# Performance work log

Hardware: AMD Instinct MI355X
Metric: run time of the kernel (lower is better)

## Reference

```python
import jax, jax.numpy as jnp
import numpy as np

TWO_PI = 2.0 * np.pi
EPS = 1e-12  # torch F.normalize eps


def setup_inputs() -> dict:
    key = jax.random.key(0)
    ks = jax.random.split(key, 12)
    B, NS, G = 16, 128, 20000
    P, S, E, T = 200, 128, 128, 50
    return {
        "x_genes": jax.random.normal(ks[0], (B, NS, G), jnp.float32),
        "tissue_idx": jax.random.randint(ks[1], (B, NS), 0, T, jnp.int32),
        "pathway_idx": jax.random.randint(ks[2], (P, S), 0, G, jnp.int32),
        "W_proj": jax.random.normal(ks[3], (P, E, S), jnp.float32) * (1.0 / np.sqrt(S)),
        "b_proj": jax.random.normal(ks[4], (P, E), jnp.float32) * 0.02,
        "tissue_table": jax.random.normal(ks[5], (T, E), jnp.float32),
        "W1": jax.random.normal(ks[6], (E, 32), jnp.float32) * (1.0 / np.sqrt(E)),
        "b1": jax.random.normal(ks[7], (32,), jnp.float32) * 0.02,
        "W2": jax.random.normal(ks[8], (32, 2), jnp.float32) * (1.0 / np.sqrt(32)),
        "b2": jax.random.normal(ks[9], (2,), jnp.float32) * 0.02,
        "Wdec": jax.random.normal(ks[10], (2, G), jnp.float32) * (1.0 / np.sqrt(2.0)),
        "bdec": jax.random.normal(ks[11], (G,), jnp.float32) * 0.02,
    }


def _l2norm(v):
    n = jnp.sqrt(jnp.sum(v * v, axis=-1, keepdims=True))
    return v / jnp.maximum(n, EPS)


def reference(x_genes, tissue_idx, pathway_idx, W_proj, b_proj, tissue_table,
              W1, b1, W2, b2, Wdec, bdec):
    B, NS, G = x_genes.shape
    x = x_genes.reshape(-1, G)            # [N, G], N = B*NS
    t = tissue_idx.reshape(-1)            # [N]

    # Pathway tokenizer: gather gene subsets + per-pathway linear (grouped GEMM)
    xg = x[:, pathway_idx]                # [N, P, S]
    H = jax.nn.relu(jnp.einsum('nps,pes->npe', xg, W_proj) + b_proj)  # [N, P, E]

    # Single-query attention with tissue embedding as query
    Q = tissue_table[t]                   # [N, E]
    scale = 1.0 / np.sqrt(H.shape[-1])
    scores = jnp.einsum('ne,npe->np', Q, H) * scale   # [N, P]
    attn = jax.nn.softmax(scores, axis=-1)
    context = jnp.einsum('np,npe->ne', attn, H)       # [N, E]

    # to_latent MLP (dropout=0 / eval)
    h = jax.nn.relu(context @ W1 + b1)
    pc = h @ W2 + b2                      # [N, 2]
    pcn = _l2norm(pc)
    ang = jnp.remainder(jnp.arctan2(pcn[:, 1], pcn[:, 0]) + TWO_PI, TWO_PI)

    # decode + normalize
    rec = _l2norm(pcn @ Wdec + bdec)      # [N, G]

    return (pcn.reshape(B, NS, 2), ang.reshape(B, NS), rec.reshape(B, NS, G))
```

## Files before the change

### kernel.cpp

```cpp
#include <hip/hip_runtime.h>
#include <cmath>

#define GG 20000
#define NN 2048
#define PP 200
#define SS 128
#define EE 128
#define TN 128
#define TPP 8
#define NOCT 25

typedef __bf16 bf16x8 __attribute__((ext_vector_type(8)));
typedef float f32x16 __attribute__((ext_vector_type(16)));
typedef unsigned short u16x8 __attribute__((ext_vector_type(8)));

__device__ __align__(16) unsigned g_xTi[(size_t)GG * NN];
__device__ __align__(16) unsigned short g_Wsw[(size_t)PP * 32768];
__device__ float g_ctxp[(size_t)NN * NOCT * EE];
__device__ float g_mT[NOCT * NN];
__device__ float g_lT[NOCT * NN];
__device__ float g_statsp[6][64];
__device__ float g_stats[8];

__device__ __forceinline__ unsigned short f2bf(float f) {
  unsigned u = __builtin_bit_cast(unsigned, f);
  return (unsigned short)((u + 0x7FFFu + ((u >> 16) & 1u)) >> 16);
}
__device__ __forceinline__ float bf2f(unsigned short h) {
  return __builtin_bit_cast(float, (unsigned)h << 16);
}
__device__ __forceinline__ unsigned packhl(float f) {
  unsigned short h = f2bf(f);
  unsigned short l = f2bf(f - bf2f(h));
  return (unsigned)h | ((unsigned)l << 16);
}

__global__ __launch_bounds__(256) void transpose_convert_kernel(
    const float* __restrict__ x)
{
  __shared__ unsigned tile[128 * 129];
  const int g0 = blockIdx.x * 128;
  const int n0 = blockIdx.y * 128;
  const int t = threadIdx.x;

  {
    const int gq = t & 31, nr = t >> 5;
    const int g = g0 + gq * 4;
    #pragma unroll
    for (int k = 0; k < 16; ++k) {
      int nl = nr + 8 * k;
      unsigned v0 = 0, v1 = 0, v2 = 0, v3 = 0;
      if (g + 3 < GG) {
        float4 v = *(const float4*)&x[(size_t)(n0 + nl) * GG + g];
        v0 = packhl(v.x); v1 = packhl(v.y); v2 = packhl(v.z); v3 = packhl(v.w);
      }
      unsigned* row = &tile[nl * 129 + gq * 4];
      row[0] = v0; row[1] = v1; row[2] = v2; row[3] = v3;
    }
  }
  __syncthreads();
  {
    const int nq = t & 31, gr = t >> 5;
    #pragma unroll
    for (int k = 0; k < 16; ++k) {
      int gl = gr + 8 * k;
      int g = g0 + gl;
      if (g < GG) {
        uint4 o;
        o.x = tile[(nq * 4 + 0) * 129 + gl];
        o.y = tile[(nq * 4 + 1) * 129 + gl];
        o.z = tile[(nq * 4 + 2) * 129 + gl];
        o.w = tile[(nq * 4 + 3) * 129 + gl];
        *(uint4*)&g_xTi[(size_t)g * NN + n0 + nq * 4] = o;
      }
    }
  }
}

__global__ __launch_bounds__(256) void wconvert_kernel(const float* __restrict__ Wp)
{
  unsigned v = blockIdx.x * 256 + threadIdx.x;
  const int si = v & 7;
  const int slp = (v >> 3) & 7;
  const int e = (v >> 6) & 127;
  const int ch = (v >> 13) & 1;
  const int p = v >> 14;
  const int slot = slp ^ (e & 7);
  const int s = ch * 64 + slot * 8 + si;
  float f = Wp[((size_t)p * EE + e) * SS + s];
  unsigned short h = f2bf(f);
  unsigned short l = f2bf(f - bf2f(h));
  size_t base = (size_t)(p * 2 + ch) * 16384 + e * 64 + slp * 8 + si;
  g_Wsw[base] = h;
  g_Wsw[base + 8192] = l;
}

__global__ __launch_bounds__(256) void wdec_stats_partial(
    const float* __restrict__ Wdec, const float* __restrict__ bdec)
{
  __shared__ float red[6][4];
  const int b = blockIdx.x;
  const int start = b * 313;
  const int end = (start + 313 < GG) ? start + 313 : GG;
  float s00 = 0, s11 = 0, s01 = 0, t0 = 0, t1 = 0, sbb = 0;
  for (int g = start + threadIdx.x; g < end; g += 256) {
    float w0 = Wdec[g], w1 = Wdec[GG + g], bb = bdec[g];
    s00 += w0 * w0; s11 += w1 * w1; s01 += w0 * w1;
    t0 += w0 * bb;  t1 += w1 * bb;  sbb += bb * bb;
  }
  #pragma unroll
  for (int off = 32; off >= 1; off >>= 1) {
    s00 += __shfl_xor(s00, off); s11 += __shfl_xor(s11, off);
    s01 += __shfl_xor(s01, off); t0 += __shfl_xor(t0, off);
    t1 += __shfl_xor(t1, off);   sbb += __shfl_xor(sbb, off);
  }
  const int w = threadIdx.x >> 6;
  if ((threadIdx.x & 63) == 0) {
    red[0][w] = s00; red[1][w] = s11; red[2][w] = s01;
    red[3][w] = t0;  red[4][w] = t1;  red[5][w] = sbb;
  }
  __syncthreads();
  if (threadIdx.x < 6)
    g_statsp[threadIdx.x][b] = red[threadIdx.x][0] + red[threadIdx.x][1] +
                               red[threadIdx.x][2] + red[threadIdx.x][3];
}

__global__ __launch_bounds__(64) void wdec_stats_final()
{
  const int t = threadIdx.x;
  #pragma unroll
  for (int k = 0; k < 6; ++k) {
    float v = g_statsp[k][t];
    #pragma unroll
    for (int off = 32; off >= 1; off >>= 1) v += __shfl_xor(v, off);
    if (t == 0) g_stats[k] = v;
  }
}

__device__ __forceinline__ void load16(unsigned* xr, const int* sidx_lds,
                                       int sbase, int kh, int ncol) {
  #pragma unroll
  for (int ks2 = 0; ks2 < 2; ++ks2)
    #pragma unroll
    for (int j = 0; j < 8; ++j) {
      int s = (sbase + ks2) * 16 + kh * 8 + j;
      xr[ks2 * 8 + j] = g_xTi[(size_t)sidx_lds[s] * NN + ncol];
    }
}

__device__ __forceinline__ void compute2ks(const unsigned short* wb,
                                           const unsigned* xr, f32x16 (&acc)[4],
                                           int ksbase, int nl, int kh) {
  #pragma unroll
  for (int ks2 = 0; ks2 < 2; ++ks2) {
    const int ks = ksbase + ks2;
    const unsigned short* wAh = wb + (ks >> 2) * 16384;
    const unsigned short* wAl = wAh + 8192;
    u16x8 bhu, blu;
    #pragma unroll
    for (int j = 0; j < 8; ++j) {
      unsigned v = xr[ks2 * 8 + j];
      bhu[j] = (unsigned short)(v & 0xffffu);
      blu[j] = (unsigned short)(v >> 16);
    }
    bf16x8 bh = __builtin_bit_cast(bf16x8, bhu);
    bf16x8 bl = __builtin_bit_cast(bf16x8, blu);
    #pragma unroll
    for (int et = 0; et < 4; ++et) {
      const int e = et * 32 + nl;
      const int slp = ((ks & 3) * 2 + kh) ^ (e & 7);
      bf16x8 ah = __builtin_bit_cast(bf16x8, *(const uint4*)(wAh + e * 64 + slp * 8));
      bf16x8 al = __builtin_bit_cast(bf16x8, *(const uint4*)(wAl + e * 64 + slp * 8));
      acc[et] = __builtin_amdgcn_mfma_f32_32x32x16_bf16(ah, bh, acc[et], 0, 0, 0);
      acc[et] = __builtin_amdgcn_mfma_f32_32x32x16_bf16(ah, bl, acc[et], 0, 0, 0);
      acc[et] = __builtin_amdgcn_mfma_f32_32x32x16_bf16(al, bh, acc[et], 0, 0, 0);
    }
  }
}

__device__ __forceinline__ void pathway_body(
    int p, unsigned short* wbuf, int* sidx, float* sbp,
    const int* __restrict__ pidx, const float* __restrict__ bp,
    const float* __restrict__ tt, int tid_n,
    int t, int w, int ln, int nl, int kh, int ncol,
    f32x16 (&h)[4], float& s_out)
{
  __syncthreads();
  if (t < 128) sidx[t] = pidx[p * SS + t];
  else         sbp[t - 128] = bp[p * EE + (t - 128)];
  {
    const unsigned short* src = g_Wsw + (size_t)p * 32768 + w * 8192 + ln * 8;
    unsigned short* dst = wbuf + w * 8192;
    #pragma unroll
    for (int j = 0; j < 16; ++j) {
      __builtin_amdgcn_global_load_lds(
          (const __attribute__((address_space(1))) unsigned int*)(src + j * 512),
          (__attribute__((address_space(3))) unsigned int*)(dst + j * 512), 16, 0, 0);
    }
  }
  __syncthreads();

  #pragma unroll
  for (int et = 0; et < 4; ++et)
    #pragma unroll
    for (int r = 0; r < 16; ++r) h[et][r] = 0.f;

  unsigned xa[16], xb[16];
  load16(xa, sidx, 0, kh, ncol);
  load16(xb, sidx, 2, kh, ncol);
  compute2ks(wbuf, xa, h, 0, nl, kh);
  load16(xa, sidx, 4, kh, ncol);
  compute2ks(wbuf, xb, h, 2, nl, kh);
  load16(xb, sidx, 6, kh, ncol);
  compute2ks(wbuf, xa, h, 4, nl, kh);
  compute2ks(wbuf, xb, h, 6, nl, kh);

  const float4* qp = (const float4*)(tt + (size_t)tid_n * EE);
  float scr = 0.f;
  #pragma unroll
  for (int et = 0; et < 4; ++et)
    #pragma unroll
    for (int rq = 0; rq < 4; ++rq) {
      int e0 = et * 32 + rq * 8 + kh * 4;
      float4 q4 = qp[e0 >> 2];
      float4 b4 = *(const float4*)&sbp[e0];
      float h0 = fmaxf(h[et][rq * 4 + 0] + b4.x, 0.f);
      float h1 = fmaxf(h[et][rq * 4 + 1] + b4.y, 0.f);
      float h2 = fmaxf(h[et][rq * 4 + 2] + b4.z, 0.f);
      float h3 = fmaxf(h[et][rq * 4 + 3] + b4.w, 0.f);
      h[et][rq * 4 + 0] = h0; h[et][rq * 4 + 1] = h1;
      h[et][rq * 4 + 2] = h2; h[et][rq * 4 + 3] = h3;
      scr += h0 * q4.x + h1 * q4.y + h2 * q4.z + h3 * q4.w;
    }
  scr += __shfl_xor(scr, 32);
  s_out = scr * 0.08838834764831845f;
}

__global__ __launch_bounds__(256, 2) void proj_mfma_kernel(
    const int* __restrict__ tidx, const int* __restrict__ pidx,
    const float* __restrict__ bp, const float* __restrict__ tt)
{
  __shared__ __align__(16) unsigned short wbuf[32768];
  __shared__ int sidx[SS];
  __shared__ float sbp[EE];

  const int t = threadIdx.x;
  const int w = t >> 6;
  const int ln = t & 63;
  const int nl = ln & 31;
  const int kh = ln >> 5;
  const int n0 = blockIdx.x * TN;
  const int oct = blockIdx.y;
  const int ncol = n0 + w * 32 + nl;
  const int tid_n = tidx[ncol];

  f32x16 ctx[4];
  #pragma unroll
  for (int et = 0; et < 4; ++et)
    #pragma unroll
    for (int r = 0; r < 16; ++r) ctx[et][r] = 0.f;
  float m_r = -1e30f, l_r = 0.f;

  f32x16 h[4];
  float s;
  for (int pp = 0; pp < TPP; ++pp) {
    pathway_body(oct * TPP + pp, wbuf, sidx, sbp, pidx, bp, tt, tid_n,
                 t, w, ln, nl, kh, ncol, h, s);
    const float mn = fmaxf(m_r, s);
    const float f = expf(m_r - mn);
    const float wg = expf(s - mn);
    l_r = l_r * f + wg;
    m_r = mn;
    #pragma unroll
    for (int et = 0; et < 4; ++et)
      #pragma unroll
      for (int r = 0; r < 16; ++r)
        ctx[et][r] = ctx[et][r] * f + wg * h[et][r];
  }

  __syncthreads();
  float* tb = ((float*)wbuf) + w * (32 * 128);
  #pragma unroll
  for (int et = 0; et < 4; ++et)
    #pragma unroll
    for (int rq = 0; rq < 4; ++rq) {
      int slot = et * 8 + rq * 2 + kh;
      float4 v = make_float4(ctx[et][rq * 4 + 0], ctx[et][rq * 4 + 1],
                             ctx[et][rq * 4 + 2], ctx[et][rq * 4 + 3]);
      *(float4*)&tb[nl * 128 + ((slot ^ nl) << 2)] = v;
    }
  __syncthreads();
  {
    const int rrow = ln >> 1, eh = (ln & 1) * 16;
    const int nn = n0 + w * 32 + rrow;
    float* dst = g_ctxp + ((size_t)nn * NOCT + oct) * EE + eh * 4;
    const float* srcrow = tb + rrow * 128;
    #pragma unroll
    for (int k = 0; k < 16; ++k) {
      int slot = eh + k;
      *(float4*)&dst[k * 4] = *(const float4*)&srcrow[(slot ^ rrow) << 2];
    }
  }
  if (ln < 32) {
    g_mT[oct * NN + ncol] = m_r;
    g_lT[oct * NN + ncol] = l_r;
  }
}

__global__ __launch_bounds__(256) void combine_rec_kernel(
    const float* __restrict__ W1, const float* __restrict__ b1,
    const float* __restrict__ W2, const float* __restrict__ b2,
    const float* __restrict__ Wdec, const float* __restrict__ bdec,
    float* __restrict__ out)
{
  const int n = blockIdx.x;
  const int t = threadIdx.x;
  __shared__ float ws[NOCT];
  __shared__ float ctx2[2][EE];
  __shared__ float r1[4], r2[4];
  __shared__ float hsh[32];
  __shared__ float qsh[3];

  float mv = (t < NOCT) ? g_mT[t * NN + n] : -1e30f;
  float lv = (t < NOCT) ? g_lT[t * NN + n] : 0.f;
  float M = mv;
  #pragma unroll
  for (int off = 32; off >= 1; off >>= 1) M = fmaxf(M, __shfl_xor(M, off));
  if ((t & 63) == 0) r1[t >> 6] = M;
  __syncthreads();
  M = fmaxf(fmaxf(r1[0], r1[1]), fmaxf(r1[2], r1[3]));
  float wv = (t < NOCT) ? expf(mv - M) : 0.f;
  if (t < NOCT) ws[t] = wv;
  float Lp = wv * lv;
  #pragma unroll
  for (int off = 32; off >= 1; off >>= 1) Lp += __shfl_xor(Lp, off);
  if ((t & 63) == 0) r2[t >> 6] = Lp;
  __syncthreads();
  const float L = r2[0] + r2[1] + r2[2] + r2[3];

  {
    const int e = t & 127, hf = t >> 7;
    const int sA = hf ? 13 : 0, sB = hf ? NOCT : 13;
    const float* base = g_ctxp + ((size_t)n * NOCT + sA) * EE + e;
    float c = 0.f;
    for (int s = sA; s < sB; ++s) c += ws[s] * base[(size_t)(s - sA) * EE];
    ctx2[hf][e] = c;
  }
  __syncthreads();
  const float invL = 1.f / L;
  if (t < 32) {
    float h = 0.f;
    for (int e = 0; e < EE; ++e) h += (ctx2[0][e] + ctx2[1][e]) * W1[e * 32 + t];
    hsh[t] = fmaxf(h * invL + b1[t], 0.f);
  }
  __syncthreads();
  if (t == 0) {
    float p0 = b2[0], p1 = b2[1];
    #pragma unroll
    for (int k = 0; k < 32; ++k) { p0 += hsh[k] * W2[k * 2]; p1 += hsh[k] * W2[k * 2 + 1]; }
    float invp = 1.f / fmaxf(sqrtf(p0 * p0 + p1 * p1), 1e-12f);
    float q0 = p0 * invp, q1 = p1 * invp;
    const float PI2 = 6.2831853071795864769f;
    float ang = atan2f(q1, q0) + PI2;
    if (ang >= PI2) ang -= PI2;
    out[n * 2 + 0] = q0;
    out[n * 2 + 1] = q1;
    out[2 * NN + n] = ang;
    float n2 = q0 * q0 * g_stats[0] + q1 * q1 * g_stats[1] +
               2.f * q0 * q1 * g_stats[2] +
               2.f * q0 * g_stats[3] + 2.f * q1 * g_stats[4] + g_stats[5];
    qsh[0] = q0;
    qsh[1] = q1;
    qsh[2] = 1.f / fmaxf(sqrtf(n2), 1e-12f);
  }
  __syncthreads();
  const float q0 = qsh[0], q1 = qsh[1], inv = qsh[2];

  float* orec = out + 3 * NN + (size_t)n * GG;
  for (int i = t; i < GG / 4; i += 256) {
    float4 w0 = *(const float4*)&Wdec[i * 4];
    float4 w1 = *(const float4*)&Wdec[GG + i * 4];
    float4 b4 = *(const float4*)&bdec[i * 4];
    float4 o;
    o.x = (q0 * w0.x + q1 * w1.x + b4.x) * inv;
    o.y = (q0 * w0.y + q1 * w1.y + b4.y) * inv;
    o.z = (q0 * w0.z + q1 * w1.z + b4.z) * inv;
    o.w = (q0 * w0.w + q1 * w1.w + b4.w) * inv;
    *(float4*)&orec[i * 4] = o;
  }
}

extern "C" void kernel_launch(void* const* d_in, const int* in_sizes, int n_in,
                              void* d_out, int out_size, void* d_ws, size_t ws_size,
                              hipStream_t stream) {
  (void)in_sizes; (void)n_in; (void)out_size; (void)d_ws; (void)ws_size;
  const float* x    = (const float*)d_in[0];
  const int*   tidx = (const int*)  d_in[1];
  const int*   pidx = (const int*)  d_in[2];
  const float* Wp   = (const float*)d_in[3];
  const float* bp   = (const float*)d_in[4];
  const float* tt   = (const float*)d_in[5];
  const float* W1   = (const float*)d_in[6];
  const float* b1   = (const float*)d_in[7];
  const float* W2   = (const float*)d_in[8];
  const float* b2   = (const float*)d_in[9];
  const float* Wdec = (const float*)d_in[10];
  const float* bdec = (const float*)d_in[11];
  float* out = (float*)d_out;

  dim3 gridT((GG + 127) / 128, NN / 128, 1);
  transpose_convert_kernel<<<gridT, 256, 0, stream>>>(x);
  wconvert_kernel<<<(PP * 16384) / 256, 256, 0, stream>>>(Wp);
  wdec_stats_partial<<<64, 256, 0, stream>>>(Wdec, bdec);
  wdec_stats_final<<<1, 64, 0, stream>>>();

  dim3 gridA(NN / TN, NOCT, 1);
  proj_mfma_kernel<<<gridA, 256, 0, stream>>>(tidx, pidx, bp, tt);

  combine_rec_kernel<<<NN, 256, 0, stream>>>(W1, b1, W2, b2, Wdec, bdec, out);
}
```

Baseline: 290.3 us.

## Halve weight LDS buffer to raise occupancy and fold stats reduction into combine

The projection kernel now stages each pathway's bf16 weights in two 32KB halves instead of one 64KB buffer. This halves LDS use so launch bounds can ask for four blocks per CU instead of two, and the context transpose is split into two phases to fit the smaller buffer. The cost is extra barriers per pathway and less overlap between the x gathers and the MFMAs. Separately, the tiny final stats-reduction kernel is removed and each combine block sums the 64 partials itself, trading one launch for redundant work in every block.

```diff
diff --git a/kernel.cpp b/kernel.cpp
--- a/kernel.cpp
+++ b/kernel.cpp
@@ -20,7 +20,6 @@
 __device__ float g_mT[NOCT * NN];
 __device__ float g_lT[NOCT * NN];
 __device__ float g_statsp[6][64];
-__device__ float g_stats[8];
 
 __device__ __forceinline__ unsigned short f2bf(float f) {
   unsigned u = __builtin_bit_cast(unsigned, f);
@@ -125,18 +124,6 @@
                                red[threadIdx.x][2] + red[threadIdx.x][3];
 }
 
-__global__ __launch_bounds__(64) void wdec_stats_final()
-{
-  const int t = threadIdx.x;
-  #pragma unroll
-  for (int k = 0; k < 6; ++k) {
-    float v = g_statsp[k][t];
-    #pragma unroll
-    for (int off = 32; off >= 1; off >>= 1) v += __shfl_xor(v, off);
-    if (t == 0) g_stats[k] = v;
-  }
-}
-
 __device__ __forceinline__ void load16(unsigned* xr, const int* sidx_lds,
                                        int sbase, int kh, int ncol) {
   #pragma unroll
@@ -150,12 +137,12 @@
 
 __device__ __forceinline__ void compute2ks(const unsigned short* wb,
                                            const unsigned* xr, f32x16 (&acc)[4],
-                                           int ksbase, int nl, int kh) {
+                                           int klbase, int nl, int kh) {
   #pragma unroll
   for (int ks2 = 0; ks2 < 2; ++ks2) {
-    const int ks = ksbase + ks2;
-    const unsigned short* wAh = wb + (ks >> 2) * 16384;
-    const unsigned short* wAl = wAh + 8192;
+    const int ksl = klbase + ks2;
+    const unsigned short* wAh = wb;
+    const unsigned short* wAl = wb + 8192;
     u16x8 bhu, blu;
     #pragma unroll
     for (int j = 0; j < 8; ++j) {
@@ -168,7 +155,7 @@
     #pragma unroll
     for (int et = 0; et < 4; ++et) {
       const int e = et * 32 + nl;
-      const int slp = ((ks & 3) * 2 + kh) ^ (e & 7);
+      const int slp = (ksl * 2 + kh) ^ (e & 7);
       bf16x8 ah = __builtin_bit_cast(bf16x8, *(const uint4*)(wAh + e * 64 + slp * 8));
       bf16x8 al = __builtin_bit_cast(bf16x8, *(const uint4*)(wAl + e * 64 + slp * 8));
       acc[et] = __builtin_amdgcn_mfma_f32_32x32x16_bf16(ah, bh, acc[et], 0, 0, 0);
@@ -185,35 +172,36 @@
     int t, int w, int ln, int nl, int kh, int ncol,
     f32x16 (&h)[4], float& s_out)
 {
-  __syncthreads();
-  if (t < 128) sidx[t] = pidx[p * SS + t];
-  else         sbp[t - 128] = bp[p * EE + (t - 128)];
-  {
-    const unsigned short* src = g_Wsw + (size_t)p * 32768 + w * 8192 + ln * 8;
-    unsigned short* dst = wbuf + w * 8192;
-    #pragma unroll
-    for (int j = 0; j < 16; ++j) {
-      __builtin_amdgcn_global_load_lds(
-          (const __attribute__((address_space(1))) unsigned int*)(src + j * 512),
-          (__attribute__((address_space(3))) unsigned int*)(dst + j * 512), 16, 0, 0);
-    }
-  }
-  __syncthreads();
-
   #pragma unroll
   for (int et = 0; et < 4; ++et)
     #pragma unroll
     for (int r = 0; r < 16; ++r) h[et][r] = 0.f;
 
-  unsigned xa[16], xb[16];
-  load16(xa, sidx, 0, kh, ncol);
-  load16(xb, sidx, 2, kh, ncol);
-  compute2ks(wbuf, xa, h, 0, nl, kh);
-  load16(xa, sidx, 4, kh, ncol);
-  compute2ks(wbuf, xb, h, 2, nl, kh);
-  load16(xb, sidx, 6, kh, ncol);
-  compute2ks(wbuf, xa, h, 4, nl, kh);
-  compute2ks(wbuf, xb, h, 6, nl, kh);
+  #pragma unroll
+  for (int ch = 0; ch < 2; ++ch) {
+    __syncthreads();
+    if (ch == 0) {
+      if (t < 128) sidx[t] = pidx[p * SS + t];
+      else         sbp[t - 128] = bp[p * EE + (t - 128)];
+    }
+    {
+      const unsigned short* src = g_Wsw + (size_t)(p * 2 + ch) * 16384 + w * 4096 + ln * 8;
+      unsigned short* dst = wbuf + w * 4096;
+      #pragma unroll
+      for (int j = 0; j < 8; ++j) {
+        __builtin_amdgcn_global_load_lds(
+            (const __attribute__((address_space(1))) unsigned int*)(src + j * 512),
+            (__attribute__((address_space(3))) unsigned int*)(dst + j * 512), 16, 0, 0);
+      }
+    }
+    __syncthreads();
+
+    unsigned xa[16], xb[16];
+    load16(xa, sidx, ch * 4 + 0, kh, ncol);
+    load16(xb, sidx, ch * 4 + 2, kh, ncol);
+    compute2ks(wbuf, xa, h, 0, nl, kh);
+    compute2ks(wbuf, xb, h, 2, nl, kh);
+  }
 
   const float4* qp = (const float4*)(tt + (size_t)tid_n * EE);
   float scr = 0.f;
@@ -236,11 +224,11 @@
   s_out = scr * 0.08838834764831845f;
 }
 
-__global__ __launch_bounds__(256, 2) void proj_mfma_kernel(
+__global__ __launch_bounds__(256, 4) void proj_mfma_kernel(
     const int* __restrict__ tidx, const int* __restrict__ pidx,
     const float* __restrict__ bp, const float* __restrict__ tt)
 {
-  __shared__ __align__(16) unsigned short wbuf[32768];
+  __shared__ __align__(16) unsigned short wbuf[16384];
   __shared__ int sidx[SS];
   __shared__ float sbp[EE];
 
@@ -279,27 +267,31 @@
   }
 
   __syncthreads();
-  float* tb = ((float*)wbuf) + w * (32 * 128);
-  #pragma unroll
-  for (int et = 0; et < 4; ++et)
-    #pragma unroll
-    for (int rq = 0; rq < 4; ++rq) {
-      int slot = et * 8 + rq * 2 + kh;
-      float4 v = make_float4(ctx[et][rq * 4 + 0], ctx[et][rq * 4 + 1],
-                             ctx[et][rq * 4 + 2], ctx[et][rq * 4 + 3]);
-      *(float4*)&tb[nl * 128 + ((slot ^ nl) << 2)] = v;
-    }
-  __syncthreads();
-  {
-    const int rrow = ln >> 1, eh = (ln & 1) * 16;
-    const int nn = n0 + w * 32 + rrow;
-    float* dst = g_ctxp + ((size_t)nn * NOCT + oct) * EE + eh * 4;
-    const float* srcrow = tb + rrow * 128;
-    #pragma unroll
-    for (int k = 0; k < 16; ++k) {
-      int slot = eh + k;
-      *(float4*)&dst[k * 4] = *(const float4*)&srcrow[(slot ^ rrow) << 2];
-    }
+  float* tbase = (float*)wbuf;
+  #pragma unroll
+  for (int ph = 0; ph < 2; ++ph) {
+    if ((w >> 1) == ph) {
+      float* tb = tbase + (w & 1) * 4096;
+      #pragma unroll
+      for (int et = 0; et < 4; ++et)
+        #pragma unroll
+        for (int rq = 0; rq < 4; ++rq) {
+          int slot = et * 8 + rq * 2 + kh;
+          float4 v = make_float4(ctx[et][rq * 4 + 0], ctx[et][rq * 4 + 1],
+                                 ctx[et][rq * 4 + 2], ctx[et][rq * 4 + 3]);
+          *(float4*)&tb[nl * 128 + ((slot ^ nl) << 2)] = v;
+        }
+      const int rrow = ln >> 1, eh = (ln & 1) * 16;
+      const int nn = n0 + w * 32 + rrow;
+      float* dst = g_ctxp + ((size_t)nn * NOCT + oct) * EE + eh * 4;
+      const float* srcrow = tb + rrow * 128;
+      #pragma unroll
+      for (int k = 0; k < 16; ++k) {
+        int slot = eh + k;
+        *(float4*)&dst[k * 4] = *(const float4*)&srcrow[(slot ^ rrow) << 2];
+      }
+    }
+    __syncthreads();
   }
   if (ln < 32) {
     g_mT[oct * NN + ncol] = m_r;
@@ -320,6 +312,14 @@
   __shared__ float r1[4], r2[4];
   __shared__ float hsh[32];
   __shared__ float qsh[3];
+  __shared__ float stats_s[6];
+
+  if (t >= 192 && t < 198) {
+    float v = 0.f;
+    #pragma unroll 8
+    for (int j = 0; j < 64; ++j) v += g_statsp[t - 192][j];
+    stats_s[t - 192] = v;
+  }
 
   float mv = (t < NOCT) ? g_mT[t * NN + n] : -1e30f;
   float lv = (t < NOCT) ? g_lT[t * NN + n] : 0.f;
@@ -366,9 +366,9 @@
     out[n * 2 + 0] = q0;
     out[n * 2 + 1] = q1;
     out[2 * NN + n] = ang;
-    float n2 = q0 * q0 * g_stats[0] + q1 * q1 * g_stats[1] +
-               2.f * q0 * q1 * g_stats[2] +
-               2.f * q0 * g_stats[3] + 2.f * q1 * g_stats[4] + g_stats[5];
+    float n2 = q0 * q0 * stats_s[0] + q1 * q1 * stats_s[1] +
+               2.f * q0 * q1 * stats_s[2] +
+               2.f * q0 * stats_s[3] + 2.f * q1 * stats_s[4] + stats_s[5];
     qsh[0] = q0;
     qsh[1] = q1;
     qsh[2] = 1.f / fmaxf(sqrtf(n2), 1e-12f);
@@ -412,7 +412,6 @@
   transpose_convert_kernel<<<gridT, 256, 0, stream>>>(x);
   wconvert_kernel<<<(PP * 16384) / 256, 256, 0, stream>>>(Wp);
   wdec_stats_partial<<<64, 256, 0, stream>>>(Wdec, bdec);
-  wdec_stats_final<<<1, 64, 0, stream>>>();
 
   dim3 gridA(NN / TN, NOCT, 1);
   proj_mfma_kernel<<<gridA, 256, 0, stream>>>(tidx, pidx, bp, tt);
```

Result: slower. 402.2 us (+38.5%).
